# Optimization experiments

Hardware: AMD Instinct MI355X
Metric: run time of the kernel (lower is better)

## Reference

```python
import jax, jax.numpy as jnp
import numpy as np

EPS = 1e-5

def bn_eval(x, p):
    # p: [4, C] = gamma, beta, running_mean, running_var; channel-last broadcast
    g, b, m, v = p[0], p[1], p[2], p[3]
    return (x - m) * (g / jnp.sqrt(v + EPS)) + b

def _bn_params(k, c):
    k1, k2, k3, k4 = jax.random.split(k, 4)
    gamma = jax.random.uniform(k1, (c,)) + 0.5
    beta = jax.random.normal(k2, (c,)) * 0.1
    mean = jax.random.normal(k3, (c,)) * 0.1
    var = jax.random.uniform(k4, (c,)) + 0.5
    return jnp.stack([gamma, beta, mean, var])

def _lin(k, fan_in, fan_out):
    bound = 1.0 / np.sqrt(fan_in)
    kw, kb = jax.random.split(k)
    w = jax.random.uniform(kw, (fan_in, fan_out), minval=-bound, maxval=bound)
    b = jax.random.uniform(kb, (fan_out,), minval=-bound, maxval=bound)
    return w, b

def setup_inputs() -> dict:
    key = jax.random.key(0)
    B, N, S, C, G = 2, 4096, 16, 256, 8
    ks = jax.random.split(key, 20)
    feats = jax.random.normal(ks[0], (B, N, C), dtype=jnp.float32)
    coords = jax.random.normal(ks[1], (B, N, 3), dtype=jnp.float32)
    index = jax.random.randint(ks[2], (B, N, S), 0, N, dtype=jnp.int32)
    wq, bq = _lin(ks[3], C, C); bnq = _bn_params(ks[4], C)
    wk, bk = _lin(ks[5], C, C); bnk = _bn_params(ks[6], C)
    wv, bv = _lin(ks[7], C, C)
    pm_w1, pm_b1 = _lin(ks[8], 3, C); pm_bn = _bn_params(ks[9], C)
    pm_w2, pm_b2 = _lin(ks[10], C, C)
    pb_w1, pb_b1 = _lin(ks[11], 3, C); pb_bn = _bn_params(ks[12], C)
    pb_w2, pb_b2 = _lin(ks[13], C, C)
    we_w1, we_b1 = _lin(ks[14], C, G); we_bn = _bn_params(ks[15], G)
    we_w2, we_b2 = _lin(ks[16], G, G)
    return dict(feats=feats, coords=coords, index=index,
                wq=wq, bq=bq, bnq=bnq, wk=wk, bk=bk, bnk=bnk, wv=wv, bv=bv,
                pm_w1=pm_w1, pm_b1=pm_b1, pm_bn=pm_bn, pm_w2=pm_w2, pm_b2=pm_b2,
                pb_w1=pb_w1, pb_b1=pb_b1, pb_bn=pb_bn, pb_w2=pb_w2, pb_b2=pb_b2,
                we_w1=we_w1, we_b1=we_b1, we_bn=we_bn, we_w2=we_w2, we_b2=we_b2)

def reference(feats, coords, index,
              wq, bq, bnq, wk, bk, bnk, wv, bv,
              pm_w1, pm_b1, pm_bn, pm_w2, pm_b2,
              pb_w1, pb_b1, pb_bn, pb_w2, pb_b2,
              we_w1, we_b1, we_bn, we_w2, we_b2):
    B, N, C = feats.shape
    S = index.shape[2]
    G = we_w1.shape[1]
    q = jax.nn.relu(bn_eval(feats @ wq + bq, bnq))                       # [B,N,C]
    k = jax.nn.relu(bn_eval(feats @ wk + bk, bnk))                       # [B,N,C]
    v = feats @ wv + bv                                                   # [B,N,C]
    idx = index.reshape(B, N * S)
    key_g = jnp.take_along_axis(k, idx[:, :, None], axis=1).reshape(B, N, S, C)
    val_g = jnp.take_along_axis(v, idx[:, :, None], axis=1).reshape(B, N, S, C)
    crd_g = jnp.take_along_axis(coords, idx[:, :, None], axis=1).reshape(B, N, S, 3)
    relation_qk = key_g - q[:, :, None, :]                                # [B,N,S,C]
    pos = coords[:, :, None, :] - crd_g                                   # [B,N,S,3]
    pem = jax.nn.relu(bn_eval(pos @ pm_w1 + pm_b1, pm_bn)) @ pm_w2 + pm_b2
    relation_qk = relation_qk * pem
    peb = jax.nn.relu(bn_eval(pos @ pb_w1 + pb_b1, pb_bn)) @ pb_w2 + pb_b2
    relation_qk = relation_qk + peb
    val_g = val_g + peb
    w = jax.nn.relu(bn_eval(relation_qk @ we_w1 + we_b1, we_bn)) @ we_w2 + we_b2  # [B,N,S,G]
    w = jax.nn.softmax(w, axis=2)                                         # softmax over neighbors
    val_g = val_g.reshape(B, N, S, G, C // G)
    out = jnp.einsum('bnsgi,bnsg->bngi', val_g, w).reshape(B, N, C)
    return out
```

## Files before the change

### kernel.cpp

```cpp
#include <hip/hip_runtime.h>
#include <hip/hip_bf16.h>


typedef __attribute__((ext_vector_type(8))) short bf16x8_t;
typedef __attribute__((ext_vector_type(4))) float f32x4_t;

#define BN_EPS 1e-5f
#define WSYNC() asm volatile("s_waitcnt lgkmcnt(0)" ::: "memory")

__device__ __forceinline__ float blo(unsigned int v) {
    union { unsigned int u; float f; } x; x.u = v << 16; return x.f;
}
__device__ __forceinline__ float bhi(unsigned int v) {
    union { unsigned int u; float f; } x; x.u = v & 0xffff0000u; return x.f;
}
__device__ __forceinline__ unsigned int fbits(float f) {
    union { float f; unsigned int u; } x; x.f = f; return x.u;
}
__device__ __forceinline__ unsigned short f2b(float f) {
    unsigned int u = fbits(f);
    return (unsigned short)((u + 0x7fffu + ((u >> 16) & 1u)) >> 16);
}
__device__ __forceinline__ float b2f(unsigned short h) {
    union { unsigned int u; float f; } x; x.u = ((unsigned int)h) << 16; return x.f;
}
__device__ __forceinline__ unsigned int f2bpk(float a, float b) {
    union { __hip_bfloat162 h; unsigned int u; } x;
    x.h = __float22bfloat162_rn(make_float2(a, b));
    return x.u;
}
__device__ __forceinline__ unsigned int relpair(unsigned int kb, unsigned int qb,
                                                unsigned int pm_, unsigned int pb_) {
    float r0 = (blo(kb) - blo(qb)) * blo(pm_) + blo(pb_);
    float r1 = (bhi(kb) - bhi(qb)) * bhi(pm_) + bhi(pb_);
    return f2bpk(r0, r1);
}

__global__ __launch_bounds__(256) void k_prep(
    const float* __restrict__ wq, const float* __restrict__ wk,
    const float* __restrict__ wv, const float* __restrict__ pm2,
    const float* __restrict__ pb2,
    const float* __restrict__ pm_w1, const float* __restrict__ pm_b1,
    const float* __restrict__ pm_bn,
    const float* __restrict__ pb_w1, const float* __restrict__ pb_b1,
    const float* __restrict__ pb_bn,
    const float* __restrict__ we_w1,
    const float* __restrict__ bq, const float* __restrict__ bnq,
    const float* __restrict__ bk, const float* __restrict__ bnk,
    const float* __restrict__ bv,
    unsigned short* __restrict__ wsT, unsigned short* __restrict__ w1F,
    unsigned short* __restrict__ we1TF, float* __restrict__ SS)
{
    const int bid = blockIdx.x, t = threadIdx.x;
    if (bid < 160) {
        __shared__ unsigned short T[32][72];
        const int mat = bid >> 5;
        const int kk  = (bid >> 2) & 7;
        const int ntq = bid & 3;
        const float* s = (mat == 0) ? wq : (mat == 1) ? wk : (mat == 2) ? wv
                         : (mat == 3) ? pm2 : pb2;
        {
            int c = t & 63, r0 = t >> 6;
            for (int i = 0; i < 8; ++i) {
                int r = r0 + i * 4;
                T[r][c] = f2b(s[(kk * 32 + r) * 256 + ntq * 64 + c]);
            }
        }
        __syncthreads();
        {
            int seg = t >> 6, lane = t & 63;
            int col = seg * 16 + (lane & 15);
            int kr  = (lane >> 4) * 8;
            unsigned int v[8];
            #pragma unroll
            for (int j = 0; j < 8; ++j) v[j] = T[kr + j][col];
            uint4 o;
            o.x = v[0] | (v[1] << 16);
            o.y = v[2] | (v[3] << 16);
            o.z = v[4] | (v[5] << 16);
            o.w = v[6] | (v[7] << 16);
            *(uint4*)(wsT + mat * 65536 + (ntq * 4 + seg) * 4096 + kk * 512 + lane * 8) = o;
        }
    } else if (bid == 160) {
        int c = t;
        int nt = c >> 4, l15 = c & 15;
        float sm = pm_bn[c] / sqrtf(pm_bn[768 + c] + BN_EPS);
        float sb = pb_bn[c] / sqrtf(pb_bn[768 + c] + BN_EPS);
        float W[2][4];
        W[0][0] = pm_w1[c] * sm; W[0][1] = pm_w1[256 + c] * sm;
        W[0][2] = pm_w1[512 + c] * sm;
        W[0][3] = (pm_b1[c] - pm_bn[512 + c]) * sm + pm_bn[256 + c];
        W[1][0] = pb_w1[c] * sb; W[1][1] = pb_w1[256 + c] * sb;
        W[1][2] = pb_w1[512 + c] * sb;
        W[1][3] = (pb_b1[c] - pb_bn[512 + c]) * sb + pb_bn[256 + c];
        for (int pass = 0; pass < 2; ++pass) {
            unsigned short xh = f2b(W[pass][0]), xl = f2b(W[pass][0] - b2f(xh));
            unsigned short yh = f2b(W[pass][1]), yl = f2b(W[pass][1] - b2f(yh));
            unsigned short zh = f2b(W[pass][2]), zl = f2b(W[pass][2] - b2f(zh));
            unsigned short bh = f2b(W[pass][3]), bl = f2b(W[pass][3] - b2f(bh));
            unsigned short sl[16] = { xh, xh, xl, yh, yh, yl, zh, zh, zl,
                                      bh, bl, 0, 0, 0, 0, 0 };
            for (int q = 0; q < 4; ++q)
                for (int j = 0; j < 8; ++j)
                    w1F[((pass * 16 + nt) * 64 + q * 16 + l15) * 8 + j] =
                        (q < 2) ? sl[q * 8 + j] : (unsigned short)0;
        }
    } else {
        for (int j = 0; j < 8; ++j) {
            int e = t * 8 + j;
            int g = e >> 8, c = e & 255;
            we1TF[g * 256 + c] = f2b(we_w1[c * 8 + g]);
        }
        int c = t;
        float sq = bnq[c] / sqrtf(bnq[768 + c] + BN_EPS);
        SS[c]        = sq;
        SS[256 + c]  = (bq[c] - bnq[512 + c]) * sq + bnq[256 + c];
        float sk = bnk[c] / sqrtf(bnk[768 + c] + BN_EPS);
        SS[512 + c]  = sk;
        SS[768 + c]  = (bk[c] - bnk[512 + c]) * sk + bnk[256 + c];
        SS[1024 + c] = 1.0f;
        SS[1280 + c] = bv[c];
    }
}

__global__ __launch_bounds__(256) void k_qkv(
    const float* __restrict__ feats,
    const unsigned short* __restrict__ wT,
    const float* __restrict__ SS,
    unsigned short* __restrict__ qkv)
{
    __shared__ unsigned short A[32][264];
    const int t    = threadIdx.x;
    const int widx = blockIdx.x >> 8;
    const int mb   = blockIdx.x & 255;

    for (int i = 0; i < 8; ++i) {
        int row = 4 * i + (t >> 6), col = (t & 63) * 4;
        float4 f = *(const float4*)(feats + (mb * 32 + row) * 256 + col);
        *(uint2*)&A[row][col] = make_uint2(f2bpk(f.x, f.y), f2bpk(f.z, f.w));
    }
    __syncthreads();

    const int lane = t & 63, w = t >> 6;
    const int ln15 = lane & 15, quad = lane >> 4;
    const int mt = w & 1, nh = w >> 1;

    bf16x8_t afr[8];
    #pragma unroll
    for (int kk = 0; kk < 8; ++kk)
        afr[kk] = *(const bf16x8_t*)&A[mt * 16 + ln15][kk * 32 + quad * 8];

    const unsigned short* W = wT + widx * 65536;
    unsigned short* dst = qkv + (size_t)widx * 8192 * 256;

    f32x4_t acc[8];
    for (int j = 0; j < 8; ++j) acc[j] = (f32x4_t){0.f, 0.f, 0.f, 0.f};

    #pragma unroll
    for (int kk = 0; kk < 8; ++kk) {
        #pragma unroll
        for (int j = 0; j < 8; ++j) {
            int nt = nh * 8 + j;
            bf16x8_t wfr = *(const bf16x8_t*)(W + ((nt * 8 + kk) * 64 + lane) * 8);
            acc[j] = __builtin_amdgcn_mfma_f32_16x16x32_bf16(wfr, afr[kk], acc[j], 0, 0, 0);
        }
    }

    const float* S = SS + widx * 512;
    const int row = mb * 32 + mt * 16 + ln15;
    #pragma unroll
    for (int j = 0; j < 8; ++j) {
        int n0 = (nh * 8 + j) * 16 + quad * 4;
        float4 s4 = *(const float4*)(S + n0);
        float4 h4 = *(const float4*)(S + 256 + n0);
        float y0 = acc[j][0] * s4.x + h4.x;
        float y1 = acc[j][1] * s4.y + h4.y;
        float y2 = acc[j][2] * s4.z + h4.z;
        float y3 = acc[j][3] * s4.w + h4.w;
        if (widx < 2) {
            y0 = fmaxf(y0, 0.f); y1 = fmaxf(y1, 0.f);
            y2 = fmaxf(y2, 0.f); y3 = fmaxf(y3, 0.f);
        }
        *(uint2*)(dst + (size_t)row * 256 + n0) =
            make_uint2(f2bpk(y0, y1), f2bpk(y2, y3));
    }
}

__global__ __launch_bounds__(512, 4) void k_main(
    const float* __restrict__ coords,
    const int*   __restrict__ index,
    const unsigned short* __restrict__ qm,
    const unsigned short* __restrict__ km,
    const unsigned short* __restrict__ vm,
    const unsigned short* __restrict__ pmw2F,
    const unsigned short* __restrict__ pbw2F,
    const unsigned short* __restrict__ w1F,
    const unsigned short* __restrict__ we1TF,
    const float* __restrict__ pm_b2, const float* __restrict__ pb_b2,
    const float* __restrict__ we_b1, const float* __restrict__ we_bn,
    const float* __restrict__ we_w2, const float* __restrict__ we_b2,
    float* __restrict__ out)
{
    __shared__ unsigned short bufR[64][264];
    __shared__ unsigned short bufP[64][264];
    __shared__ unsigned short posX[64][32];
    __shared__ float us_[8][16][10];
    __shared__ float we2s[8][8];
    __shared__ float web2[8], swe8[8], dwe8[8];

    const int t   = threadIdx.x;
    const int P0  = blockIdx.x * 4;
    const int bb_ = P0 >> 12;
    const int w = t >> 6, lane = t & 63;
    const int ln15 = lane & 15, quad = lane >> 4;
    const int p   = w >> 1, sub = w & 1;
    const int R0  = p * 16;
    const int Pg  = P0 + p;

    const int rg = (bb_ << 12) + index[Pg * 16 + ln15];

    if (t < 64) {
        int m  = t;
        int Pr = P0 + (m >> 4);
        int rs = (bb_ << 12) + index[Pr * 16 + (m & 15)];
        float x = coords[Pr * 3 + 0] - coords[rs * 3 + 0];
        float y = coords[Pr * 3 + 1] - coords[rs * 3 + 1];
        float z = coords[Pr * 3 + 2] - coords[rs * 3 + 2];
        unsigned short xh = f2b(x), xl = f2b(x - b2f(xh));
        unsigned short yh = f2b(y), yl = f2b(y - b2f(yh));
        unsigned short zh = f2b(z), zl = f2b(z - b2f(zh));
        const unsigned short one = 0x3f80;
        posX[m][0] = xh; posX[m][1] = xl; posX[m][2] = xh;
        posX[m][3] = yh; posX[m][4] = yl; posX[m][5] = yh;
        posX[m][6] = zh; posX[m][7] = zl; posX[m][8] = zh;
        posX[m][9] = one; posX[m][10] = one;
        #pragma unroll
        for (int j2 = 11; j2 < 32; ++j2) posX[m][j2] = 0;
        we2s[m >> 3][m & 7] = we_w2[m];
    }
    if (t < 8) {
        float s = we_bn[t] / sqrtf(we_bn[24 + t] + BN_EPS);
        swe8[t] = s;
        dwe8[t] = (we_b1[t] - we_bn[16 + t]) * s + we_bn[8 + t];
        web2[t] = we_b2[t];
    }
    __syncthreads();

    bf16x8_t afrP[4];
    #pragma unroll
    for (int mt = 0; mt < 4; ++mt)
        afrP[mt] = *(const bf16x8_t*)&posX[mt * 16 + ln15][quad * 8];

    {
        f32x4_t hb[2][4];
        for (int ntl = 0; ntl < 2; ++ntl)
            for (int mt = 0; mt < 4; ++mt) hb[ntl][mt] = (f32x4_t){0.f, 0.f, 0.f, 0.f};
        #pragma unroll
        for (int ntl = 0; ntl < 2; ++ntl) {
            int nt = w * 2 + ntl;
            bf16x8_t wfr = *(const bf16x8_t*)(w1F + ((16 + nt) * 64 + lane) * 8);
            #pragma unroll
            for (int mt = 0; mt < 4; ++mt)
                hb[ntl][mt] = __builtin_amdgcn_mfma_f32_16x16x32_bf16(wfr, afrP[mt], hb[ntl][mt], 0, 0, 0);
        }
        #pragma unroll
        for (int ntl = 0; ntl < 2; ++ntl) {
            int cb = w * 32 + ntl * 16 + quad * 4;
            #pragma unroll
            for (int mt = 0; mt < 4; ++mt) {
                unsigned int pk0 = f2bpk(fmaxf(hb[ntl][mt][0], 0.f), fmaxf(hb[ntl][mt][1], 0.f));
                unsigned int pk1 = f2bpk(fmaxf(hb[ntl][mt][2], 0.f), fmaxf(hb[ntl][mt][3], 0.f));
                *(uint2*)&bufR[mt * 16 + ln15][cb] = make_uint2(pk0, pk1);
            }
        }
    }
    __syncthreads();

    f32x4_t accM[2][4];
    for (int ntl = 0; ntl < 2; ++ntl)
        for (int mt = 0; mt < 4; ++mt) accM[ntl][mt] = (f32x4_t){0.f, 0.f, 0.f, 0.f};
    #pragma unroll
    for (int ntl = 0; ntl < 2; ++ntl) {
        int nt = w * 2 + ntl;
        bf16x8_t wfr = *(const bf16x8_t*)(w1F + (nt * 64 + lane) * 8);
        #pragma unroll
        for (int mt = 0; mt < 4; ++mt)
            accM[ntl][mt] = __builtin_amdgcn_mfma_f32_16x16x32_bf16(wfr, afrP[mt], accM[ntl][mt], 0, 0, 0);
    }
    f32x4_t acc[2][4];
    {
        f32x4_t b0 = *(const f32x4_t*)(pb_b2 + (w * 2    ) * 16 + quad * 4);
        f32x4_t b1 = *(const f32x4_t*)(pb_b2 + (w * 2 + 1) * 16 + quad * 4);
        for (int mt = 0; mt < 4; ++mt) { acc[0][mt] = b0; acc[1][mt] = b1; }
    }
    #pragma unroll
    for (int kk = 0; kk < 8; ++kk) {
        bf16x8_t afr[4];
        #pragma unroll
        for (int mt = 0; mt < 4; ++mt)
            afr[mt] = *(const bf16x8_t*)&bufR[mt * 16 + ln15][kk * 32 + quad * 8];
        #pragma unroll
        for (int ntl = 0; ntl < 2; ++ntl) {
            int nt = w * 2 + ntl;
            bf16x8_t wfr = *(const bf16x8_t*)(pbw2F + ((nt * 8 + kk) * 64 + lane) * 8);
            #pragma unroll
            for (int mt = 0; mt < 4; ++mt)
                acc[ntl][mt] = __builtin_amdgcn_mfma_f32_16x16x32_bf16(wfr, afr[mt], acc[ntl][mt], 0, 0, 0);
        }
    }
    #pragma unroll
    for (int ntl = 0; ntl < 2; ++ntl) {
        int cb = w * 32 + ntl * 16 + quad * 4;
        #pragma unroll
        for (int mt = 0; mt < 4; ++mt) {
            unsigned int pk0 = f2bpk(acc[ntl][mt][0], acc[ntl][mt][1]);
            unsigned int pk1 = f2bpk(acc[ntl][mt][2], acc[ntl][mt][3]);
            *(uint2*)&bufP[mt * 16 + ln15][cb] = make_uint2(pk0, pk1);
        }
    }
    __syncthreads();

    #pragma unroll
    for (int ntl = 0; ntl < 2; ++ntl) {
        int cb = w * 32 + ntl * 16 + quad * 4;
        #pragma unroll
        for (int mt = 0; mt < 4; ++mt) {
            unsigned int pk0 = f2bpk(fmaxf(accM[ntl][mt][0], 0.f), fmaxf(accM[ntl][mt][1], 0.f));
            unsigned int pk1 = f2bpk(fmaxf(accM[ntl][mt][2], 0.f), fmaxf(accM[ntl][mt][3], 0.f));
            *(uint2*)&bufR[mt * 16 + ln15][cb] = make_uint2(pk0, pk1);
        }
    }
    __syncthreads();

    uint4 kpre[8];
    #pragma unroll
    for (int kk = 0; kk < 8; ++kk)
        kpre[kk] = *(const uint4*)(km + (size_t)rg * 256 + kk * 32 + quad * 8);
    {
        f32x4_t b0 = *(const f32x4_t*)(pm_b2 + (w * 2    ) * 16 + quad * 4);
        f32x4_t b1 = *(const f32x4_t*)(pm_b2 + (w * 2 + 1) * 16 + quad * 4);
        for (int mt = 0; mt < 4; ++mt) { acc[0][mt] = b0; acc[1][mt] = b1; }
    }
    #pragma unroll
    for (int kk = 0; kk < 8; ++kk) {
        bf16x8_t afr[4];
        #pragma unroll
        for (int mt = 0; mt < 4; ++mt)
            afr[mt] = *(const bf16x8_t*)&bufR[mt * 16 + ln15][kk * 32 + quad * 8];
        #pragma unroll
        for (int ntl = 0; ntl < 2; ++ntl) {
            int nt = w * 2 + ntl;
            bf16x8_t wfr = *(const bf16x8_t*)(pmw2F + ((nt * 8 + kk) * 64 + lane) * 8);
            #pragma unroll
            for (int mt = 0; mt < 4; ++mt)
                acc[ntl][mt] = __builtin_amdgcn_mfma_f32_16x16x32_bf16(wfr, afr[mt], acc[ntl][mt], 0, 0, 0);
        }
    }
    __syncthreads();

    uint4 qpre[8];
    #pragma unroll
    for (int kk = 0; kk < 8; ++kk)
        qpre[kk] = *(const uint4*)(qm + (size_t)Pg * 256 + kk * 32 + quad * 8);
    const int c5 = (sub * 64 + lane) * 2;
    unsigned int vpre[16];
    #pragma unroll
    for (int s = 0; s < 16; ++s) {
        int rv = __shfl(rg, s);
        vpre[s] = *(const unsigned int*)(vm + (size_t)rv * 256 + c5);
    }

    #pragma unroll
    for (int ntl = 0; ntl < 2; ++ntl) {
        int cb = w * 32 + ntl * 16 + quad * 4;
        #pragma unroll
        for (int mt = 0; mt < 4; ++mt) {
            unsigned int pk0 = f2bpk(acc[ntl][mt][0], acc[ntl][mt][1]);
            unsigned int pk1 = f2bpk(acc[ntl][mt][2], acc[ntl][mt][3]);
            *(uint2*)&bufR[mt * 16 + ln15][cb] = make_uint2(pk0, pk1);
        }
    }
    __syncthreads();

    {
        const bf16x8_t bz = {0, 0, 0, 0, 0, 0, 0, 0};
        f32x4_t lacc = {0.f, 0.f, 0.f, 0.f};
        #pragma unroll
        for (int kk = 0; kk < 8; ++kk) {
            int cb8 = kk * 32 + quad * 8;
            uint4 pm4 = *(const uint4*)&bufR[R0 + ln15][cb8];
            uint4 pb4 = *(const uint4*)&bufP[R0 + ln15][cb8];
            uint4 q4  = qpre[kk];
            union { uint4 u; bf16x8_t v; } rr;
            rr.u.x = relpair(kpre[kk].x, q4.x, pm4.x, pb4.x);
            rr.u.y = relpair(kpre[kk].y, q4.y, pm4.y, pb4.y);
            rr.u.z = relpair(kpre[kk].z, q4.z, pm4.z, pb4.z);
            rr.u.w = relpair(kpre[kk].w, q4.w, pm4.w, pb4.w);
            bf16x8_t wfr = bz;
            if (ln15 < 8) wfr = *(const bf16x8_t*)(we1TF + ln15 * 256 + cb8);
            lacc = __builtin_amdgcn_mfma_f32_16x16x32_bf16(wfr, rr.v, lacc, 0, 0, 0);
        }
        if (quad < 2) {
            f32x4_t uv4;
            #pragma unroll
            for (int r = 0; r < 4; ++r) {
                int g = quad * 4 + r;
                uv4[r] = fmaxf(lacc[r] * swe8[g] + dwe8[g], 0.f);
            }
            *(f32x4_t*)&us_[w][ln15][quad * 4] = uv4;
        }
    }
    WSYNC();

    if (lane < 16) {
        int s = lane;
        float uvv[8], l[8];
        #pragma unroll
        for (int g = 0; g < 8; ++g) uvv[g] = us_[w][s][g];
        #pragma unroll
        for (int g = 0; g < 8; ++g) {
            float x = web2[g];
            for (int gp = 0; gp < 8; ++gp) x += uvv[gp] * we2s[gp][g];
            l[g] = x;
        }
        #pragma unroll
        for (int g = 0; g < 8; ++g) us_[w][s][g] = l[g];
    }
    WSYNC();

    if (lane < 8) {
        int g = lane;
        float mx = -1e30f;
        for (int s = 0; s < 16; ++s) mx = fmaxf(mx, us_[w][s][g]);
        float e[16], sum = 0.f;
        for (int s = 0; s < 16; ++s) { e[s] = __expf(us_[w][s][g] - mx); sum += e[s]; }
        float inv = 1.f / sum;
        for (int s = 0; s < 16; ++s) us_[w][s][g] = e[s] * inv;
    }
    WSYNC();

    {
        int g = c5 >> 5;
        float a0 = 0.f, a1 = 0.f;
        #pragma unroll
        for (int s = 0; s < 16; ++s) {
            float wv_ = us_[w][s][g];
            unsigned int v2 = vpre[s];
            unsigned int p2 = *(const unsigned int*)&bufP[R0 + s][c5];
            a0 += wv_ * (blo(v2) + blo(p2));
            a1 += wv_ * (bhi(v2) + bhi(p2));
        }
        *(float2*)(out + (size_t)Pg * 256 + c5) = make_float2(a0, a1);
    }
}

extern "C" void kernel_launch(void* const* d_in, const int* in_sizes, int n_in,
                              void* d_out, int out_size, void* d_ws, size_t ws_size,
                              hipStream_t stream)
{
    const float* feats  = (const float*)d_in[0];
    const float* coords = (const float*)d_in[1];
    const int*   index  = (const int*)d_in[2];
    const float* wq     = (const float*)d_in[3];
    const float* bq     = (const float*)d_in[4];
    const float* bnq    = (const float*)d_in[5];
    const float* wk     = (const float*)d_in[6];
    const float* bk     = (const float*)d_in[7];
    const float* bnk    = (const float*)d_in[8];
    const float* wv     = (const float*)d_in[9];
    const float* bv     = (const float*)d_in[10];
    const float* pm_w1  = (const float*)d_in[11];
    const float* pm_b1  = (const float*)d_in[12];
    const float* pm_bn  = (const float*)d_in[13];
    const float* pm_w2  = (const float*)d_in[14];
    const float* pm_b2  = (const float*)d_in[15];
    const float* pb_w1  = (const float*)d_in[16];
    const float* pb_b1  = (const float*)d_in[17];
    const float* pb_bn  = (const float*)d_in[18];
    const float* pb_w2  = (const float*)d_in[19];
    const float* pb_b2  = (const float*)d_in[20];
    const float* we_w1  = (const float*)d_in[21];
    const float* we_b1  = (const float*)d_in[22];
    const float* we_bn  = (const float*)d_in[23];
    const float* we_w2  = (const float*)d_in[24];
    const float* we_b2  = (const float*)d_in[25];

    unsigned short* qkv   = (unsigned short*)d_ws;
    unsigned short* wsT   = qkv + (size_t)3 * 8192 * 256;
    unsigned short* we1TF = wsT + 5 * 65536;
    unsigned short* w1F   = we1TF + 2048;
    float*          SS    = (float*)(w1F + 16384);

    const size_t need = (size_t)13281280;
    if (ws_size < need) {
        hipMemsetAsync(d_out, 0, (size_t)out_size * 4, stream);
        return;
    }

    k_prep<<<162,  256, 0, stream>>>(wq, wk, wv, pm_w2, pb_w2,
                                     pm_w1, pm_b1, pm_bn,
                                     pb_w1, pb_b1, pb_bn,
                                     we_w1,
                                     bq, bnq, bk, bnk, bv,
                                     wsT, w1F, we1TF, SS);
    k_qkv <<<768,  256, 0, stream>>>(feats, wsT, SS, qkv);
    k_main<<<2048, 512, 0, stream>>>(coords, index,
                                     qkv,
                                     qkv + (size_t)8192 * 256,
                                     qkv + (size_t)2 * 8192 * 256,
                                     wsT + 3 * 65536,
                                     wsT + 4 * 65536,
                                     w1F, we1TF,
                                     pm_b2, pb_b2,
                                     we_b1, we_bn, we_w2, we_b2,
                                     (float*)d_out);
}
```

Measured before the change: 212.4 us.

## Give each wavefront a full point in k_main, removing block barriers

Restructures k_main from 512-thread blocks, where 8 waves split columns across 4 points with __syncthreads, to 256-thread blocks where each wave owns one point and computes all 256 output columns. Inter-wave barriers become wave-local LDS waits. Weight fragments are now loaded per wave rather than shared across the block's points. The we BN scale and bias precompute moves into k_prep, and the final reduction uses wider vector loads and stores. The trade is more global weight traffic per point and more registers per wave in exchange for no block-level synchronisation.

```diff
diff --git a/kernel.cpp b/kernel.cpp
--- a/kernel.cpp
+++ b/kernel.cpp
@@ -48,6 +48,8 @@
     const float* __restrict__ bq, const float* __restrict__ bnq,
     const float* __restrict__ bk, const float* __restrict__ bnk,
     const float* __restrict__ bv,
+    const float* __restrict__ we_b1, const float* __restrict__ we_bn,
+    const float* __restrict__ we_b2,
     unsigned short* __restrict__ wsT, unsigned short* __restrict__ w1F,
     unsigned short* __restrict__ we1TF, float* __restrict__ SS)
 {
@@ -120,6 +122,12 @@
         SS[768 + c]  = (bk[c] - bnk[512 + c]) * sk + bnk[256 + c];
         SS[1024 + c] = 1.0f;
         SS[1280 + c] = bv[c];
+        if (t < 8) {
+            float s = we_bn[t] / sqrtf(we_bn[24 + t] + BN_EPS);
+            SS[1536 + t] = s;
+            SS[1544 + t] = (we_b1[t] - we_bn[16 + t]) * s + we_bn[8 + t];
+            SS[1552 + t] = we_b2[t];
+        }
     }
 }
 
@@ -186,7 +194,7 @@
     }
 }
 
-__global__ __launch_bounds__(512, 4) void k_main(
+__global__ __launch_bounds__(256, 2) void k_main(
     const float* __restrict__ coords,
     const int*   __restrict__ index,
     const unsigned short* __restrict__ qm,
@@ -197,205 +205,138 @@
     const unsigned short* __restrict__ w1F,
     const unsigned short* __restrict__ we1TF,
     const float* __restrict__ pm_b2, const float* __restrict__ pb_b2,
-    const float* __restrict__ we_b1, const float* __restrict__ we_bn,
-    const float* __restrict__ we_w2, const float* __restrict__ we_b2,
+    const float* __restrict__ we_w2, const float* __restrict__ SSE,
     float* __restrict__ out)
 {
-    __shared__ unsigned short bufR[64][264];
-    __shared__ unsigned short bufP[64][264];
-    __shared__ unsigned short posX[64][32];
-    __shared__ float us_[8][16][10];
-    __shared__ float we2s[8][8];
-    __shared__ float web2[8], swe8[8], dwe8[8];
-
-    const int t   = threadIdx.x;
-    const int P0  = blockIdx.x * 4;
-    const int bb_ = P0 >> 12;
+    __shared__ unsigned short posX[4][16][32];
+    __shared__ unsigned short bufR[4][16][264];
+    __shared__ unsigned short bufP[4][16][264];
+    __shared__ float us_[4][16][12];
+
+    const int t = threadIdx.x;
     const int w = t >> 6, lane = t & 63;
     const int ln15 = lane & 15, quad = lane >> 4;
-    const int p   = w >> 1, sub = w & 1;
-    const int R0  = p * 16;
-    const int Pg  = P0 + p;
-
-    const int rg = (bb_ << 12) + index[Pg * 16 + ln15];
-
-    if (t < 64) {
-        int m  = t;
-        int Pr = P0 + (m >> 4);
-        int rs = (bb_ << 12) + index[Pr * 16 + (m & 15)];
-        float x = coords[Pr * 3 + 0] - coords[rs * 3 + 0];
-        float y = coords[Pr * 3 + 1] - coords[rs * 3 + 1];
-        float z = coords[Pr * 3 + 2] - coords[rs * 3 + 2];
+    const int Pg  = blockIdx.x * 4 + w;
+    const int bb_ = Pg >> 12;
+    const int rg  = (bb_ << 12) + index[Pg * 16 + ln15];
+
+    if (lane < 16) {
+        int m  = lane;
+        int rs = (bb_ << 12) + index[Pg * 16 + m];
+        float x = coords[Pg * 3 + 0] - coords[rs * 3 + 0];
+        float y = coords[Pg * 3 + 1] - coords[rs * 3 + 1];
+        float z = coords[Pg * 3 + 2] - coords[rs * 3 + 2];
         unsigned short xh = f2b(x), xl = f2b(x - b2f(xh));
         unsigned short yh = f2b(y), yl = f2b(y - b2f(yh));
         unsigned short zh = f2b(z), zl = f2b(z - b2f(zh));
         const unsigned short one = 0x3f80;
-        posX[m][0] = xh; posX[m][1] = xl; posX[m][2] = xh;
-        posX[m][3] = yh; posX[m][4] = yl; posX[m][5] = yh;
-        posX[m][6] = zh; posX[m][7] = zl; posX[m][8] = zh;
-        posX[m][9] = one; posX[m][10] = one;
-        #pragma unroll
-        for (int j2 = 11; j2 < 32; ++j2) posX[m][j2] = 0;
-        we2s[m >> 3][m & 7] = we_w2[m];
-    }
-    if (t < 8) {
-        float s = we_bn[t] / sqrtf(we_bn[24 + t] + BN_EPS);
-        swe8[t] = s;
-        dwe8[t] = (we_b1[t] - we_bn[16 + t]) * s + we_bn[8 + t];
-        web2[t] = we_b2[t];
-    }
-    __syncthreads();
-
-    bf16x8_t afrP[4];
-    #pragma unroll
-    for (int mt = 0; mt < 4; ++mt)
-        afrP[mt] = *(const bf16x8_t*)&posX[mt * 16 + ln15][quad * 8];
-
-    {
-        f32x4_t hb[2][4];
-        for (int ntl = 0; ntl < 2; ++ntl)
-            for (int mt = 0; mt < 4; ++mt) hb[ntl][mt] = (f32x4_t){0.f, 0.f, 0.f, 0.f};
-        #pragma unroll
-        for (int ntl = 0; ntl < 2; ++ntl) {
-            int nt = w * 2 + ntl;
-            bf16x8_t wfr = *(const bf16x8_t*)(w1F + ((16 + nt) * 64 + lane) * 8);
-            #pragma unroll
-            for (int mt = 0; mt < 4; ++mt)
-                hb[ntl][mt] = __builtin_amdgcn_mfma_f32_16x16x32_bf16(wfr, afrP[mt], hb[ntl][mt], 0, 0, 0);
-        }
-        #pragma unroll
-        for (int ntl = 0; ntl < 2; ++ntl) {
-            int cb = w * 32 + ntl * 16 + quad * 4;
-            #pragma unroll
-            for (int mt = 0; mt < 4; ++mt) {
-                unsigned int pk0 = f2bpk(fmaxf(hb[ntl][mt][0], 0.f), fmaxf(hb[ntl][mt][1], 0.f));
-                unsigned int pk1 = f2bpk(fmaxf(hb[ntl][mt][2], 0.f), fmaxf(hb[ntl][mt][3], 0.f));
-                *(uint2*)&bufR[mt * 16 + ln15][cb] = make_uint2(pk0, pk1);
-            }
-        }
-    }
-    __syncthreads();
-
-    f32x4_t accM[2][4];
-    for (int ntl = 0; ntl < 2; ++ntl)
-        for (int mt = 0; mt < 4; ++mt) accM[ntl][mt] = (f32x4_t){0.f, 0.f, 0.f, 0.f};
-    #pragma unroll
-    for (int ntl = 0; ntl < 2; ++ntl) {
-        int nt = w * 2 + ntl;
+        posX[w][m][0] = xh; posX[w][m][1] = xl; posX[w][m][2] = xh;
+        posX[w][m][3] = yh; posX[w][m][4] = yl; posX[w][m][5] = yh;
+        posX[w][m][6] = zh; posX[w][m][7] = zl; posX[w][m][8] = zh;
+        posX[w][m][9] = one; posX[w][m][10] = one;
+        #pragma unroll
+        for (int j2 = 11; j2 < 32; ++j2) posX[w][m][j2] = 0;
+    }
+    WSYNC();
+
+    const bf16x8_t afrP = *(const bf16x8_t*)&posX[w][ln15][quad * 8];
+    const f32x4_t zz = (f32x4_t){0.f, 0.f, 0.f, 0.f};
+
+    f32x4_t hacc[16];
+    #pragma unroll
+    for (int nt = 0; nt < 16; ++nt) {
+        bf16x8_t wfr = *(const bf16x8_t*)(w1F + ((16 + nt) * 64 + lane) * 8);
+        hacc[nt] = __builtin_amdgcn_mfma_f32_16x16x32_bf16(wfr, afrP, zz, 0, 0, 0);
+    }
+    #pragma unroll
+    for (int nt = 0; nt < 16; ++nt) {
+        unsigned int pk0 = f2bpk(fmaxf(hacc[nt][0], 0.f), fmaxf(hacc[nt][1], 0.f));
+        unsigned int pk1 = f2bpk(fmaxf(hacc[nt][2], 0.f), fmaxf(hacc[nt][3], 0.f));
+        *(uint2*)&bufR[w][ln15][nt * 16 + quad * 4] = make_uint2(pk0, pk1);
+    }
+    WSYNC();
+
+    bf16x8_t hfr[8];
+    #pragma unroll
+    for (int kk = 0; kk < 8; ++kk)
+        hfr[kk] = *(const bf16x8_t*)&bufR[w][ln15][kk * 32 + quad * 8];
+    f32x4_t acc[16];
+    #pragma unroll
+    for (int nt = 0; nt < 16; ++nt)
+        acc[nt] = *(const f32x4_t*)(pb_b2 + nt * 16 + quad * 4);
+    #pragma unroll
+    for (int kk = 0; kk < 8; ++kk) {
+        #pragma unroll
+        for (int nt = 0; nt < 16; ++nt) {
+            bf16x8_t wfr = *(const bf16x8_t*)(pbw2F + ((nt * 8 + kk) * 64 + lane) * 8);
+            acc[nt] = __builtin_amdgcn_mfma_f32_16x16x32_bf16(wfr, hfr[kk], acc[nt], 0, 0, 0);
+        }
+    }
+    #pragma unroll
+    for (int nt = 0; nt < 16; ++nt) {
+        unsigned int pk0 = f2bpk(acc[nt][0], acc[nt][1]);
+        unsigned int pk1 = f2bpk(acc[nt][2], acc[nt][3]);
+        *(uint2*)&bufP[w][ln15][nt * 16 + quad * 4] = make_uint2(pk0, pk1);
+    }
+
+    #pragma unroll
+    for (int nt = 0; nt < 16; ++nt) {
         bf16x8_t wfr = *(const bf16x8_t*)(w1F + (nt * 64 + lane) * 8);
-        #pragma unroll
-        for (int mt = 0; mt < 4; ++mt)
-            accM[ntl][mt] = __builtin_amdgcn_mfma_f32_16x16x32_bf16(wfr, afrP[mt], accM[ntl][mt], 0, 0, 0);
-    }
-    f32x4_t acc[2][4];
-    {
-        f32x4_t b0 = *(const f32x4_t*)(pb_b2 + (w * 2    ) * 16 + quad * 4);
-        f32x4_t b1 = *(const f32x4_t*)(pb_b2 + (w * 2 + 1) * 16 + quad * 4);
-        for (int mt = 0; mt < 4; ++mt) { acc[0][mt] = b0; acc[1][mt] = b1; }
-    }
+        hacc[nt] = __builtin_amdgcn_mfma_f32_16x16x32_bf16(wfr, afrP, zz, 0, 0, 0);
+    }
+    WSYNC();
+    #pragma unroll
+    for (int nt = 0; nt < 16; ++nt) {
+        unsigned int pk0 = f2bpk(fmaxf(hacc[nt][0], 0.f), fmaxf(hacc[nt][1], 0.f));
+        unsigned int pk1 = f2bpk(fmaxf(hacc[nt][2], 0.f), fmaxf(hacc[nt][3], 0.f));
+        *(uint2*)&bufR[w][ln15][nt * 16 + quad * 4] = make_uint2(pk0, pk1);
+    }
+    WSYNC();
+
+    bf16x8_t hfr2[8];
+    #pragma unroll
+    for (int kk = 0; kk < 8; ++kk)
+        hfr2[kk] = *(const bf16x8_t*)&bufR[w][ln15][kk * 32 + quad * 8];
+    #pragma unroll
+    for (int nt = 0; nt < 16; ++nt)
+        acc[nt] = *(const f32x4_t*)(pm_b2 + nt * 16 + quad * 4);
     #pragma unroll
     for (int kk = 0; kk < 8; ++kk) {
-        bf16x8_t afr[4];
-        #pragma unroll
-        for (int mt = 0; mt < 4; ++mt)
-            afr[mt] = *(const bf16x8_t*)&bufR[mt * 16 + ln15][kk * 32 + quad * 8];
-        #pragma unroll
-        for (int ntl = 0; ntl < 2; ++ntl) {
-            int nt = w * 2 + ntl;
-            bf16x8_t wfr = *(const bf16x8_t*)(pbw2F + ((nt * 8 + kk) * 64 + lane) * 8);
-            #pragma unroll
-            for (int mt = 0; mt < 4; ++mt)
-                acc[ntl][mt] = __builtin_amdgcn_mfma_f32_16x16x32_bf16(wfr, afr[mt], acc[ntl][mt], 0, 0, 0);
-        }
-    }
-    #pragma unroll
-    for (int ntl = 0; ntl < 2; ++ntl) {
-        int cb = w * 32 + ntl * 16 + quad * 4;
-        #pragma unroll
-        for (int mt = 0; mt < 4; ++mt) {
-            unsigned int pk0 = f2bpk(acc[ntl][mt][0], acc[ntl][mt][1]);
-            unsigned int pk1 = f2bpk(acc[ntl][mt][2], acc[ntl][mt][3]);
-            *(uint2*)&bufP[mt * 16 + ln15][cb] = make_uint2(pk0, pk1);
-        }
-    }
-    __syncthreads();
-
-    #pragma unroll
-    for (int ntl = 0; ntl < 2; ++ntl) {
-        int cb = w * 32 + ntl * 16 + quad * 4;
-        #pragma unroll
-        for (int mt = 0; mt < 4; ++mt) {
-            unsigned int pk0 = f2bpk(fmaxf(accM[ntl][mt][0], 0.f), fmaxf(accM[ntl][mt][1], 0.f));
-            unsigned int pk1 = f2bpk(fmaxf(accM[ntl][mt][2], 0.f), fmaxf(accM[ntl][mt][3], 0.f));
-            *(uint2*)&bufR[mt * 16 + ln15][cb] = make_uint2(pk0, pk1);
-        }
-    }
-    __syncthreads();
-
-    uint4 kpre[8];
-    #pragma unroll
-    for (int kk = 0; kk < 8; ++kk)
+        #pragma unroll
+        for (int nt = 0; nt < 16; ++nt) {
+            bf16x8_t wfr = *(const bf16x8_t*)(pmw2F + ((nt * 8 + kk) * 64 + lane) * 8);
+            acc[nt] = __builtin_amdgcn_mfma_f32_16x16x32_bf16(wfr, hfr2[kk], acc[nt], 0, 0, 0);
+        }
+    }
+
+    uint4 kpre[8], qpre[8];
+    #pragma unroll
+    for (int kk = 0; kk < 8; ++kk) {
         kpre[kk] = *(const uint4*)(km + (size_t)rg * 256 + kk * 32 + quad * 8);
-    {
-        f32x4_t b0 = *(const f32x4_t*)(pm_b2 + (w * 2    ) * 16 + quad * 4);
-        f32x4_t b1 = *(const f32x4_t*)(pm_b2 + (w * 2 + 1) * 16 + quad * 4);
-        for (int mt = 0; mt < 4; ++mt) { acc[0][mt] = b0; acc[1][mt] = b1; }
-    }
-    #pragma unroll
-    for (int kk = 0; kk < 8; ++kk) {
-        bf16x8_t afr[4];
-        #pragma unroll
-        for (int mt = 0; mt < 4; ++mt)
-            afr[mt] = *(const bf16x8_t*)&bufR[mt * 16 + ln15][kk * 32 + quad * 8];
-        #pragma unroll
-        for (int ntl = 0; ntl < 2; ++ntl) {
-            int nt = w * 2 + ntl;
-            bf16x8_t wfr = *(const bf16x8_t*)(pmw2F + ((nt * 8 + kk) * 64 + lane) * 8);
-            #pragma unroll
-            for (int mt = 0; mt < 4; ++mt)
-                acc[ntl][mt] = __builtin_amdgcn_mfma_f32_16x16x32_bf16(wfr, afr[mt], acc[ntl][mt], 0, 0, 0);
-        }
-    }
-    __syncthreads();
-
-    uint4 qpre[8];
-    #pragma unroll
-    for (int kk = 0; kk < 8; ++kk)
         qpre[kk] = *(const uint4*)(qm + (size_t)Pg * 256 + kk * 32 + quad * 8);
-    const int c5 = (sub * 64 + lane) * 2;
-    unsigned int vpre[16];
-    #pragma unroll
-    for (int s = 0; s < 16; ++s) {
-        int rv = __shfl(rg, s);
-        vpre[s] = *(const unsigned int*)(vm + (size_t)rv * 256 + c5);
-    }
-
-    #pragma unroll
-    for (int ntl = 0; ntl < 2; ++ntl) {
-        int cb = w * 32 + ntl * 16 + quad * 4;
-        #pragma unroll
-        for (int mt = 0; mt < 4; ++mt) {
-            unsigned int pk0 = f2bpk(acc[ntl][mt][0], acc[ntl][mt][1]);
-            unsigned int pk1 = f2bpk(acc[ntl][mt][2], acc[ntl][mt][3]);
-            *(uint2*)&bufR[mt * 16 + ln15][cb] = make_uint2(pk0, pk1);
-        }
-    }
-    __syncthreads();
+    }
+
+    #pragma unroll
+    for (int nt = 0; nt < 16; ++nt) {
+        unsigned int pk0 = f2bpk(acc[nt][0], acc[nt][1]);
+        unsigned int pk1 = f2bpk(acc[nt][2], acc[nt][3]);
+        *(uint2*)&bufR[w][ln15][nt * 16 + quad * 4] = make_uint2(pk0, pk1);
+    }
+    WSYNC();
 
     {
         const bf16x8_t bz = {0, 0, 0, 0, 0, 0, 0, 0};
-        f32x4_t lacc = {0.f, 0.f, 0.f, 0.f};
+        f32x4_t lacc = zz;
         #pragma unroll
         for (int kk = 0; kk < 8; ++kk) {
             int cb8 = kk * 32 + quad * 8;
-            uint4 pm4 = *(const uint4*)&bufR[R0 + ln15][cb8];
-            uint4 pb4 = *(const uint4*)&bufP[R0 + ln15][cb8];
-            uint4 q4  = qpre[kk];
+            uint4 pm4 = *(const uint4*)&bufR[w][ln15][cb8];
+            uint4 pb4 = *(const uint4*)&bufP[w][ln15][cb8];
             union { uint4 u; bf16x8_t v; } rr;
-            rr.u.x = relpair(kpre[kk].x, q4.x, pm4.x, pb4.x);
-            rr.u.y = relpair(kpre[kk].y, q4.y, pm4.y, pb4.y);
-            rr.u.z = relpair(kpre[kk].z, q4.z, pm4.z, pb4.z);
-            rr.u.w = relpair(kpre[kk].w, q4.w, pm4.w, pb4.w);
+            rr.u.x = relpair(kpre[kk].x, qpre[kk].x, pm4.x, pb4.x);
+            rr.u.y = relpair(kpre[kk].y, qpre[kk].y, pm4.y, pb4.y);
+            rr.u.z = relpair(kpre[kk].z, qpre[kk].z, pm4.z, pb4.z);
+            rr.u.w = relpair(kpre[kk].w, qpre[kk].w, pm4.w, pb4.w);
             bf16x8_t wfr = bz;
             if (ln15 < 8) wfr = *(const bf16x8_t*)(we1TF + ln15 * 256 + cb8);
             lacc = __builtin_amdgcn_mfma_f32_16x16x32_bf16(wfr, rr.v, lacc, 0, 0, 0);
@@ -405,10 +346,18 @@
             #pragma unroll
             for (int r = 0; r < 4; ++r) {
                 int g = quad * 4 + r;
-                uv4[r] = fmaxf(lacc[r] * swe8[g] + dwe8[g], 0.f);
+                uv4[r] = fmaxf(lacc[r] * SSE[g] + SSE[8 + g], 0.f);
             }
             *(f32x4_t*)&us_[w][ln15][quad * 4] = uv4;
         }
+    }
+
+    const int c4 = lane * 4;
+    uint2 vpre[16];
+    #pragma unroll
+    for (int s = 0; s < 16; ++s) {
+        int rv = __shfl(rg, s);
+        vpre[s] = *(const uint2*)(vm + (size_t)rv * 256 + c4);
     }
     WSYNC();
 
@@ -419,8 +368,9 @@
         for (int g = 0; g < 8; ++g) uvv[g] = us_[w][s][g];
         #pragma unroll
         for (int g = 0; g < 8; ++g) {
-            float x = web2[g];
-            for (int gp = 0; gp < 8; ++gp) x += uvv[gp] * we2s[gp][g];
+            float x = SSE[16 + g];
+            #pragma unroll
+            for (int gp = 0; gp < 8; ++gp) x += uvv[gp] * we_w2[gp * 8 + g];
             l[g] = x;
         }
         #pragma unroll
@@ -440,17 +390,19 @@
     WSYNC();
 
     {
-        int g = c5 >> 5;
-        float a0 = 0.f, a1 = 0.f;
+        int g = lane >> 3;
+        float a0 = 0.f, a1 = 0.f, a2 = 0.f, a3 = 0.f;
         #pragma unroll
         for (int s = 0; s < 16; ++s) {
             float wv_ = us_[w][s][g];
-            unsigned int v2 = vpre[s];
-            unsigned int p2 = *(const unsigned int*)&bufP[R0 + s][c5];
-            a0 += wv_ * (blo(v2) + blo(p2));
-            a1 += wv_ * (bhi(v2) + bhi(p2));
-        }
-        *(float2*)(out + (size_t)Pg * 256 + c5) = make_float2(a0, a1);
+            uint2 v2 = vpre[s];
+            uint2 p2 = *(const uint2*)&bufP[w][s][c4];
+            a0 += wv_ * (blo(v2.x) + blo(p2.x));
+            a1 += wv_ * (bhi(v2.x) + bhi(p2.x));
+            a2 += wv_ * (blo(v2.y) + blo(p2.y));
+            a3 += wv_ * (bhi(v2.y) + bhi(p2.y));
+        }
+        *(float4*)(out + (size_t)Pg * 256 + c4) = make_float4(a0, a1, a2, a3);
     }
 }
 
@@ -491,7 +443,7 @@
     unsigned short* w1F   = we1TF + 2048;
     float*          SS    = (float*)(w1F + 16384);
 
-    const size_t need = (size_t)13281280;
+    const size_t need = (size_t)13281376;
     if (ws_size < need) {
         hipMemsetAsync(d_out, 0, (size_t)out_size * 4, stream);
         return;
@@ -502,9 +454,10 @@
                                      pb_w1, pb_b1, pb_bn,
                                      we_w1,
                                      bq, bnq, bk, bnk, bv,
+                                     we_b1, we_bn, we_b2,
                                      wsT, w1F, we1TF, SS);
     k_qkv <<<768,  256, 0, stream>>>(feats, wsT, SS, qkv);
-    k_main<<<2048, 512, 0, stream>>>(coords, index,
+    k_main<<<2048, 256, 0, stream>>>(coords, index,
                                      qkv,
                                      qkv + (size_t)8192 * 256,
                                      qkv + (size_t)2 * 8192 * 256,
@@ -512,6 +465,6 @@
                                      wsT + 4 * 65536,
                                      w1F, we1TF,
                                      pm_b2, pb_b2,
-                                     we_b1, we_bn, we_w2, we_b2,
+                                     we_w2, SS + 1536,
                                      (float*)d_out);
 }
```

Result: slower. 269.2 us (+26.8%).

## Repartition MFMA work per wave to cut register footprint and split relation dot

Applied to the files above, without the earlier changes.

Each wave now computes 4 column tiles over 2 row tiles instead of 2 column tiles over 4 row tiles. This halves the position-fragment registers and shares each weight fragment across fewer MFMAs. The relation/we1 reduction is split across the two sub-waves over K halves, with partial sums combined in shared memory after a block barrier, which halves the kpre/qpre prefetch registers. Value gathers are no longer prefetched into registers but loaded directly in the final loop using row indices cached in shared memory. The aim is lower register pressure and better occupancy, at the cost of extra barriers and less latency hiding for the value gather.

```diff
diff --git a/kernel.cpp b/kernel.cpp
--- a/kernel.cpp
+++ b/kernel.cpp
@@ -204,7 +204,9 @@
     __shared__ unsigned short bufR[64][264];
     __shared__ unsigned short bufP[64][264];
     __shared__ unsigned short posX[64][32];
-    __shared__ float us_[8][16][10];
+    __shared__ float usP[2][64][8];
+    __shared__ float us_[64][8];
+    __shared__ int   rowg_[64];
     __shared__ float we2s[8][8];
     __shared__ float web2[8], swe8[8], dwe8[8];
 
@@ -223,6 +225,7 @@
         int m  = t;
         int Pr = P0 + (m >> 4);
         int rs = (bb_ << 12) + index[Pr * 16 + (m & 15)];
+        rowg_[m] = rs;
         float x = coords[Pr * 3 + 0] - coords[rs * 3 + 0];
         float y = coords[Pr * 3 + 1] - coords[rs * 3 + 1];
         float z = coords[Pr * 3 + 2] - coords[rs * 3 + 2];
@@ -246,148 +249,130 @@
     }
     __syncthreads();
 
-    bf16x8_t afrP[4];
-    #pragma unroll
-    for (int mt = 0; mt < 4; ++mt)
-        afrP[mt] = *(const bf16x8_t*)&posX[mt * 16 + ln15][quad * 8];
+    bf16x8_t afrP[2];
+    #pragma unroll
+    for (int i = 0; i < 2; ++i)
+        afrP[i] = *(const bf16x8_t*)&posX[(sub * 2 + i) * 16 + ln15][quad * 8];
+    const f32x4_t zz = (f32x4_t){0.f, 0.f, 0.f, 0.f};
 
     {
-        f32x4_t hb[2][4];
-        for (int ntl = 0; ntl < 2; ++ntl)
-            for (int mt = 0; mt < 4; ++mt) hb[ntl][mt] = (f32x4_t){0.f, 0.f, 0.f, 0.f};
-        #pragma unroll
-        for (int ntl = 0; ntl < 2; ++ntl) {
-            int nt = w * 2 + ntl;
-            bf16x8_t wfr = *(const bf16x8_t*)(w1F + ((16 + nt) * 64 + lane) * 8);
+        f32x4_t hb[4][2];
+        #pragma unroll
+        for (int j = 0; j < 4; ++j) {
+            bf16x8_t wfr = *(const bf16x8_t*)(w1F + ((16 + p * 4 + j) * 64 + lane) * 8);
             #pragma unroll
-            for (int mt = 0; mt < 4; ++mt)
-                hb[ntl][mt] = __builtin_amdgcn_mfma_f32_16x16x32_bf16(wfr, afrP[mt], hb[ntl][mt], 0, 0, 0);
-        }
-        #pragma unroll
-        for (int ntl = 0; ntl < 2; ++ntl) {
-            int cb = w * 32 + ntl * 16 + quad * 4;
+            for (int i = 0; i < 2; ++i)
+                hb[j][i] = __builtin_amdgcn_mfma_f32_16x16x32_bf16(wfr, afrP[i], zz, 0, 0, 0);
+        }
+        #pragma unroll
+        for (int j = 0; j < 4; ++j)
             #pragma unroll
-            for (int mt = 0; mt < 4; ++mt) {
-                unsigned int pk0 = f2bpk(fmaxf(hb[ntl][mt][0], 0.f), fmaxf(hb[ntl][mt][1], 0.f));
-                unsigned int pk1 = f2bpk(fmaxf(hb[ntl][mt][2], 0.f), fmaxf(hb[ntl][mt][3], 0.f));
-                *(uint2*)&bufR[mt * 16 + ln15][cb] = make_uint2(pk0, pk1);
+            for (int i = 0; i < 2; ++i) {
+                unsigned int pk0 = f2bpk(fmaxf(hb[j][i][0], 0.f), fmaxf(hb[j][i][1], 0.f));
+                unsigned int pk1 = f2bpk(fmaxf(hb[j][i][2], 0.f), fmaxf(hb[j][i][3], 0.f));
+                *(uint2*)&bufR[(sub * 2 + i) * 16 + ln15][(p * 4 + j) * 16 + quad * 4] =
+                    make_uint2(pk0, pk1);
             }
-        }
-    }
-    __syncthreads();
-
-    f32x4_t accM[2][4];
-    for (int ntl = 0; ntl < 2; ++ntl)
-        for (int mt = 0; mt < 4; ++mt) accM[ntl][mt] = (f32x4_t){0.f, 0.f, 0.f, 0.f};
-    #pragma unroll
-    for (int ntl = 0; ntl < 2; ++ntl) {
-        int nt = w * 2 + ntl;
-        bf16x8_t wfr = *(const bf16x8_t*)(w1F + (nt * 64 + lane) * 8);
-        #pragma unroll
-        for (int mt = 0; mt < 4; ++mt)
-            accM[ntl][mt] = __builtin_amdgcn_mfma_f32_16x16x32_bf16(wfr, afrP[mt], accM[ntl][mt], 0, 0, 0);
-    }
-    f32x4_t acc[2][4];
-    {
-        f32x4_t b0 = *(const f32x4_t*)(pb_b2 + (w * 2    ) * 16 + quad * 4);
-        f32x4_t b1 = *(const f32x4_t*)(pb_b2 + (w * 2 + 1) * 16 + quad * 4);
-        for (int mt = 0; mt < 4; ++mt) { acc[0][mt] = b0; acc[1][mt] = b1; }
+    }
+    __syncthreads();
+
+    f32x4_t accM[4][2];
+    #pragma unroll
+    for (int j = 0; j < 4; ++j) {
+        bf16x8_t wfr = *(const bf16x8_t*)(w1F + ((p * 4 + j) * 64 + lane) * 8);
+        #pragma unroll
+        for (int i = 0; i < 2; ++i)
+            accM[j][i] = __builtin_amdgcn_mfma_f32_16x16x32_bf16(wfr, afrP[i], zz, 0, 0, 0);
+    }
+    f32x4_t acc[4][2];
+    #pragma unroll
+    for (int j = 0; j < 4; ++j) {
+        f32x4_t b = *(const f32x4_t*)(pb_b2 + (p * 4 + j) * 16 + quad * 4);
+        acc[j][0] = b; acc[j][1] = b;
     }
     #pragma unroll
     for (int kk = 0; kk < 8; ++kk) {
-        bf16x8_t afr[4];
-        #pragma unroll
-        for (int mt = 0; mt < 4; ++mt)
-            afr[mt] = *(const bf16x8_t*)&bufR[mt * 16 + ln15][kk * 32 + quad * 8];
-        #pragma unroll
-        for (int ntl = 0; ntl < 2; ++ntl) {
-            int nt = w * 2 + ntl;
-            bf16x8_t wfr = *(const bf16x8_t*)(pbw2F + ((nt * 8 + kk) * 64 + lane) * 8);
+        bf16x8_t hfr[2];
+        #pragma unroll
+        for (int i = 0; i < 2; ++i)
+            hfr[i] = *(const bf16x8_t*)&bufR[(sub * 2 + i) * 16 + ln15][kk * 32 + quad * 8];
+        #pragma unroll
+        for (int j = 0; j < 4; ++j) {
+            bf16x8_t wfr = *(const bf16x8_t*)(pbw2F + (((p * 4 + j) * 8 + kk) * 64 + lane) * 8);
             #pragma unroll
-            for (int mt = 0; mt < 4; ++mt)
-                acc[ntl][mt] = __builtin_amdgcn_mfma_f32_16x16x32_bf16(wfr, afr[mt], acc[ntl][mt], 0, 0, 0);
-        }
-    }
-    #pragma unroll
-    for (int ntl = 0; ntl < 2; ++ntl) {
-        int cb = w * 32 + ntl * 16 + quad * 4;
-        #pragma unroll
-        for (int mt = 0; mt < 4; ++mt) {
-            unsigned int pk0 = f2bpk(acc[ntl][mt][0], acc[ntl][mt][1]);
-            unsigned int pk1 = f2bpk(acc[ntl][mt][2], acc[ntl][mt][3]);
-            *(uint2*)&bufP[mt * 16 + ln15][cb] = make_uint2(pk0, pk1);
-        }
-    }
-    __syncthreads();
-
-    #pragma unroll
-    for (int ntl = 0; ntl < 2; ++ntl) {
-        int cb = w * 32 + ntl * 16 + quad * 4;
-        #pragma unroll
-        for (int mt = 0; mt < 4; ++mt) {
-            unsigned int pk0 = f2bpk(fmaxf(accM[ntl][mt][0], 0.f), fmaxf(accM[ntl][mt][1], 0.f));
-            unsigned int pk1 = f2bpk(fmaxf(accM[ntl][mt][2], 0.f), fmaxf(accM[ntl][mt][3], 0.f));
-            *(uint2*)&bufR[mt * 16 + ln15][cb] = make_uint2(pk0, pk1);
-        }
-    }
-    __syncthreads();
-
-    uint4 kpre[8];
-    #pragma unroll
-    for (int kk = 0; kk < 8; ++kk)
-        kpre[kk] = *(const uint4*)(km + (size_t)rg * 256 + kk * 32 + quad * 8);
-    {
-        f32x4_t b0 = *(const f32x4_t*)(pm_b2 + (w * 2    ) * 16 + quad * 4);
-        f32x4_t b1 = *(const f32x4_t*)(pm_b2 + (w * 2 + 1) * 16 + quad * 4);
-        for (int mt = 0; mt < 4; ++mt) { acc[0][mt] = b0; acc[1][mt] = b1; }
+            for (int i = 0; i < 2; ++i)
+                acc[j][i] = __builtin_amdgcn_mfma_f32_16x16x32_bf16(wfr, hfr[i], acc[j][i], 0, 0, 0);
+        }
+    }
+    #pragma unroll
+    for (int j = 0; j < 4; ++j)
+        #pragma unroll
+        for (int i = 0; i < 2; ++i) {
+            unsigned int pk0 = f2bpk(acc[j][i][0], acc[j][i][1]);
+            unsigned int pk1 = f2bpk(acc[j][i][2], acc[j][i][3]);
+            *(uint2*)&bufP[(sub * 2 + i) * 16 + ln15][(p * 4 + j) * 16 + quad * 4] =
+                make_uint2(pk0, pk1);
+        }
+    __syncthreads();
+
+    #pragma unroll
+    for (int j = 0; j < 4; ++j)
+        #pragma unroll
+        for (int i = 0; i < 2; ++i) {
+            unsigned int pk0 = f2bpk(fmaxf(accM[j][i][0], 0.f), fmaxf(accM[j][i][1], 0.f));
+            unsigned int pk1 = f2bpk(fmaxf(accM[j][i][2], 0.f), fmaxf(accM[j][i][3], 0.f));
+            *(uint2*)&bufR[(sub * 2 + i) * 16 + ln15][(p * 4 + j) * 16 + quad * 4] =
+                make_uint2(pk0, pk1);
+        }
+    __syncthreads();
+
+    uint4 kpre[4];
+    #pragma unroll
+    for (int kk = 0; kk < 4; ++kk)
+        kpre[kk] = *(const uint4*)(km + (size_t)rg * 256 + (sub * 4 + kk) * 32 + quad * 8);
+    #pragma unroll
+    for (int j = 0; j < 4; ++j) {
+        f32x4_t b = *(const f32x4_t*)(pm_b2 + (p * 4 + j) * 16 + quad * 4);
+        acc[j][0] = b; acc[j][1] = b;
     }
     #pragma unroll
     for (int kk = 0; kk < 8; ++kk) {
-        bf16x8_t afr[4];
-        #pragma unroll
-        for (int mt = 0; mt < 4; ++mt)
-            afr[mt] = *(const bf16x8_t*)&bufR[mt * 16 + ln15][kk * 32 + quad * 8];
-        #pragma unroll
-        for (int ntl = 0; ntl < 2; ++ntl) {
-            int nt = w * 2 + ntl;
-            bf16x8_t wfr = *(const bf16x8_t*)(pmw2F + ((nt * 8 + kk) * 64 + lane) * 8);
+        bf16x8_t hfr[2];
+        #pragma unroll
+        for (int i = 0; i < 2; ++i)
+            hfr[i] = *(const bf16x8_t*)&bufR[(sub * 2 + i) * 16 + ln15][kk * 32 + quad * 8];
+        #pragma unroll
+        for (int j = 0; j < 4; ++j) {
+            bf16x8_t wfr = *(const bf16x8_t*)(pmw2F + (((p * 4 + j) * 8 + kk) * 64 + lane) * 8);
             #pragma unroll
-            for (int mt = 0; mt < 4; ++mt)
-                acc[ntl][mt] = __builtin_amdgcn_mfma_f32_16x16x32_bf16(wfr, afr[mt], acc[ntl][mt], 0, 0, 0);
-        }
-    }
-    __syncthreads();
-
-    uint4 qpre[8];
-    #pragma unroll
-    for (int kk = 0; kk < 8; ++kk)
-        qpre[kk] = *(const uint4*)(qm + (size_t)Pg * 256 + kk * 32 + quad * 8);
-    const int c5 = (sub * 64 + lane) * 2;
-    unsigned int vpre[16];
-    #pragma unroll
-    for (int s = 0; s < 16; ++s) {
-        int rv = __shfl(rg, s);
-        vpre[s] = *(const unsigned int*)(vm + (size_t)rv * 256 + c5);
-    }
-
-    #pragma unroll
-    for (int ntl = 0; ntl < 2; ++ntl) {
-        int cb = w * 32 + ntl * 16 + quad * 4;
-        #pragma unroll
-        for (int mt = 0; mt < 4; ++mt) {
-            unsigned int pk0 = f2bpk(acc[ntl][mt][0], acc[ntl][mt][1]);
-            unsigned int pk1 = f2bpk(acc[ntl][mt][2], acc[ntl][mt][3]);
-            *(uint2*)&bufR[mt * 16 + ln15][cb] = make_uint2(pk0, pk1);
-        }
-    }
+            for (int i = 0; i < 2; ++i)
+                acc[j][i] = __builtin_amdgcn_mfma_f32_16x16x32_bf16(wfr, hfr[i], acc[j][i], 0, 0, 0);
+        }
+    }
+    __syncthreads();
+
+    uint4 qpre[4];
+    #pragma unroll
+    for (int kk = 0; kk < 4; ++kk)
+        qpre[kk] = *(const uint4*)(qm + (size_t)Pg * 256 + (sub * 4 + kk) * 32 + quad * 8);
+
+    #pragma unroll
+    for (int j = 0; j < 4; ++j)
+        #pragma unroll
+        for (int i = 0; i < 2; ++i) {
+            unsigned int pk0 = f2bpk(acc[j][i][0], acc[j][i][1]);
+            unsigned int pk1 = f2bpk(acc[j][i][2], acc[j][i][3]);
+            *(uint2*)&bufR[(sub * 2 + i) * 16 + ln15][(p * 4 + j) * 16 + quad * 4] =
+                make_uint2(pk0, pk1);
+        }
     __syncthreads();
 
     {
         const bf16x8_t bz = {0, 0, 0, 0, 0, 0, 0, 0};
         f32x4_t lacc = {0.f, 0.f, 0.f, 0.f};
         #pragma unroll
-        for (int kk = 0; kk < 8; ++kk) {
-            int cb8 = kk * 32 + quad * 8;
+        for (int kk = 0; kk < 4; ++kk) {
+            int cb8 = (sub * 4 + kk) * 32 + quad * 8;
             uint4 pm4 = *(const uint4*)&bufR[R0 + ln15][cb8];
             uint4 pb4 = *(const uint4*)&bufP[R0 + ln15][cb8];
             uint4 q4  = qpre[kk];
@@ -400,52 +385,50 @@
             if (ln15 < 8) wfr = *(const bf16x8_t*)(we1TF + ln15 * 256 + cb8);
             lacc = __builtin_amdgcn_mfma_f32_16x16x32_bf16(wfr, rr.v, lacc, 0, 0, 0);
         }
-        if (quad < 2) {
-            f32x4_t uv4;
-            #pragma unroll
-            for (int r = 0; r < 4; ++r) {
-                int g = quad * 4 + r;
-                uv4[r] = fmaxf(lacc[r] * swe8[g] + dwe8[g], 0.f);
-            }
-            *(f32x4_t*)&us_[w][ln15][quad * 4] = uv4;
-        }
-    }
-    WSYNC();
-
-    if (lane < 16) {
+        if (quad < 2)
+            *(f32x4_t*)&usP[sub][R0 + ln15][quad * 4] = lacc;
+    }
+    __syncthreads();
+
+    if (sub == 0 && lane < 16) {
         int s = lane;
-        float uvv[8], l[8];
-        #pragma unroll
-        for (int g = 0; g < 8; ++g) uvv[g] = us_[w][s][g];
+        float uv[8], l[8];
+        #pragma unroll
+        for (int g = 0; g < 8; ++g) {
+            float x = usP[0][R0 + s][g] + usP[1][R0 + s][g];
+            uv[g] = fmaxf(x * swe8[g] + dwe8[g], 0.f);
+        }
         #pragma unroll
         for (int g = 0; g < 8; ++g) {
             float x = web2[g];
-            for (int gp = 0; gp < 8; ++gp) x += uvv[gp] * we2s[gp][g];
+            for (int gp = 0; gp < 8; ++gp) x += uv[gp] * we2s[gp][g];
             l[g] = x;
         }
         #pragma unroll
-        for (int g = 0; g < 8; ++g) us_[w][s][g] = l[g];
+        for (int g = 0; g < 8; ++g) us_[R0 + s][g] = l[g];
     }
     WSYNC();
 
-    if (lane < 8) {
+    if (sub == 0 && lane < 8) {
         int g = lane;
         float mx = -1e30f;
-        for (int s = 0; s < 16; ++s) mx = fmaxf(mx, us_[w][s][g]);
+        for (int s = 0; s < 16; ++s) mx = fmaxf(mx, us_[R0 + s][g]);
         float e[16], sum = 0.f;
-        for (int s = 0; s < 16; ++s) { e[s] = __expf(us_[w][s][g] - mx); sum += e[s]; }
+        for (int s = 0; s < 16; ++s) { e[s] = __expf(us_[R0 + s][g] - mx); sum += e[s]; }
         float inv = 1.f / sum;
-        for (int s = 0; s < 16; ++s) us_[w][s][g] = e[s] * inv;
-    }
-    WSYNC();
+        for (int s = 0; s < 16; ++s) us_[R0 + s][g] = e[s] * inv;
+    }
+    __syncthreads();
 
     {
-        int g = c5 >> 5;
+        int idx2 = sub * 64 + lane;
+        int c5 = idx2 * 2, g = c5 >> 5;
         float a0 = 0.f, a1 = 0.f;
         #pragma unroll
         for (int s = 0; s < 16; ++s) {
-            float wv_ = us_[w][s][g];
-            unsigned int v2 = vpre[s];
+            int rv = rowg_[R0 + s];
+            float wv_ = us_[R0 + s][g];
+            unsigned int v2 = *(const unsigned int*)(vm + (size_t)rv * 256 + c5);
             unsigned int p2 = *(const unsigned int*)&bufP[R0 + s][c5];
             a0 += wv_ * (blo(v2) + blo(p2));
             a1 += wv_ * (bhi(v2) + bhi(p2));
```

New measurement: 212.3 us. Within noise of the previous version (-0.0%).
